# Optimization experiments

Measured on AMD Instinct MI355X. Metric: run time of the kernel, lower is better.

The kernel has to match this reference:

```python
import jax, jax.numpy as jnp
import numpy as np

RNN = 1024     # rnn_size
POSE = 135     # config.pose_size (15 joints x 3x3 rotmat)
SEED = 120     # seed_seq_len
TGT = 24       # target_seq_len
B = 256        # batch size


def setup_inputs() -> dict:
    key = jax.random.key(0)
    k0, k1, k2, k3, k4 = jax.random.split(key, 5)
    s = 1.0 / np.sqrt(RNN)
    poses = jax.random.normal(k0, (B, SEED + TGT, POSE), dtype=jnp.float32)
    # nn.LSTMCell(input_size, rnn_size, bias=False): weights U(-1/sqrt(H), 1/sqrt(H))
    W_ih = jax.random.uniform(k1, (4 * RNN, POSE), minval=-s, maxval=s, dtype=jnp.float32)
    W_hh = jax.random.uniform(k2, (4 * RNN, RNN), minval=-s, maxval=s, dtype=jnp.float32)
    # nn.Linear(rnn_size, pose_size)
    W_fc = jax.random.uniform(k3, (POSE, RNN), minval=-s, maxval=s, dtype=jnp.float32)
    b_fc = jax.random.uniform(k4, (POSE,), minval=-s, maxval=s, dtype=jnp.float32)
    return {"poses": poses, "W_ih": W_ih, "W_hh": W_hh, "W_fc": W_fc, "b_fc": b_fc}


def reference(poses, W_ih, W_hh, W_fc, b_fc):
    def cell(x, h, c):
        # PyTorch LSTMCell gate order: i, f, g, o ; bias=False
        gates = x @ W_ih.T + h @ W_hh.T          # [B, 4*RNN]
        i, f, g, o = jnp.split(gates, 4, axis=-1)
        c_new = jax.nn.sigmoid(f) * c + jax.nn.sigmoid(i) * jnp.tanh(g)
        h_new = jax.nn.sigmoid(o) * jnp.tanh(c_new)
        return h_new, c_new

    # Encoder: steps over poses[:, 0:SEED-1] (dropout p=0 -> identity)
    enc_inputs = jnp.transpose(poses[:, : SEED - 1], (1, 0, 2))  # [SEED-1, B, POSE]
    h0 = jnp.zeros((B, RNN), dtype=poses.dtype)
    c0 = jnp.zeros((B, RNN), dtype=poses.dtype)

    def enc_step(carry, x):
        h, c = carry
        h, c = cell(x, h, c)
        return (h, c), None

    (h, c), _ = jax.lax.scan(enc_step, (h0, c0), enc_inputs)

    # first decoder input (poses[:, SEED-1]) is ground truth. inp is detached.
    inp0 = poses[:, SEED - 1]  # [B, POSE]

    def dec_step(carry, _):
        h, c, inp = carry
        inp = jax.lax.stop_gradient(inp)  # inp.detach() in the original
        h, c = cell(inp, h, c)
        out = inp + h @ W_fc.T + b_fc     # residual + linear decode
        return (h, c, out), out

    _, outs = jax.lax.scan(dec_step, (h, c, inp0), None, length=TGT)  # [TGT, B, POSE]
    return jnp.transpose(outs, (1, 0, 2))  # predictions [B, TGT, POSE]
```

## Files before the change

### kernel.cpp

```cpp
#include <hip/hip_runtime.h>
#include <stdint.h>

#define NB 256
#define NH 1024
#define NPOSE 135
#define NPPAD 160
#define NSTEPS 143
#define NDEC 24
#define KTOT 1184
#define LSTR 168
#define NWG 256

typedef __bf16 bf16;
typedef __attribute__((ext_vector_type(8))) __bf16 bf16x8;
typedef __attribute__((ext_vector_type(4))) float f32x4;
typedef __attribute__((ext_vector_type(4))) uint32_t u32x4;

#define WCAT_OFF 0
#define WCAT_BYTES (4096l * KTOT * 2)
#define WFC_OFF  (WCAT_OFF + WCAT_BYTES)
#define WFC_BYTES (144l * 1024 * 2)
#define X_OFF    (WFC_OFF + WFC_BYTES)
#define X_BYTES  (143l * NB * NPPAD * 2)
#define H_OFF    (X_OFF + X_BYTES)
#define H_BYTES2    (2l * NB * NH * 2)
#define H_BYTES144  (144l * NB * NH * 2)
#define BAR_BYTES 16384

__device__ __forceinline__ u32x4 llc_ld16(const void* p) {
  u32x4 v;
  asm volatile("global_load_dwordx4 %0, %1, off sc0 sc1"
               : "=v"(v) : "v"(p) : "memory");
  return v;
}
__device__ __forceinline__ uint32_t llc_ld4(const void* p) {
  uint32_t v;
  asm volatile("global_load_dword %0, %1, off sc0 sc1"
               : "=v"(v) : "v"(p) : "memory");
  return v;
}
__device__ __forceinline__ u32x4 g_ld16(const void* p) {
  u32x4 v;
  asm volatile("global_load_dwordx4 %0, %1, off"
               : "=v"(v) : "v"(p) : "memory");
  return v;
}
__device__ __forceinline__ u32x4 ld16sel(const void* p, bool cached) {
  return cached ? g_ld16(p) : llc_ld16(p);
}
__device__ __forceinline__ void llc_st2(void* p, uint32_t v) {
  asm volatile("global_store_short %0, %1, off sc0 sc1"
               :: "v"(p), "v"(v) : "memory");
}
#define WAIT_VM(n) do { \
    asm volatile("s_waitcnt vmcnt(" #n ")" ::: "memory"); \
    __builtin_amdgcn_sched_barrier(0); } while (0)

#define POLL(ptr, tgt) do { \
    while (__hip_atomic_load((ptr), __ATOMIC_RELAXED, __HIP_MEMORY_SCOPE_AGENT) < (tgt)) \
      __builtin_amdgcn_s_sleep(1); \
  } while (0)
#define POLL_ALL8(tgt) do { \
    for (;;) { \
      int v_ = __hip_atomic_load(&bar[(bb * 8 + (lane & 7)) * 32], \
                                 __ATOMIC_RELAXED, __HIP_MEMORY_SCOPE_AGENT); \
      if (__all(v_ >= (tgt))) break; \
      __builtin_amdgcn_s_sleep(1); \
    } } while (0)
#define POLL01(tgt) do { \
    for (;;) { \
      int v_ = __hip_atomic_load(&bar[(bb * 8 + (lane & 1)) * 32], \
                                 __ATOMIC_RELAXED, __HIP_MEMORY_SCOPE_AGENT); \
      if (__all(v_ >= (tgt))) break; \
      __builtin_amdgcn_s_sleep(1); \
    } } while (0)
#define CHK(fv, ch, tgt) do { \
    while ((int)(fv) < (tgt)) { \
      __builtin_amdgcn_s_sleep(1); \
      fv = llc_ld4(&bar[(bb * 8 + (ch)) * 32]); \
      WAIT_VM(0); \
    } } while (0)

__global__ void k_zero(uint32_t* p, int n) {
  int i = blockIdx.x * blockDim.x + threadIdx.x;
  int st = gridDim.x * blockDim.x;
  for (; i < n; i += st) p[i] = 0u;
}

__global__ void k_wcat(const float* __restrict__ Whh, const float* __restrict__ Wih,
                       bf16* __restrict__ W) {
  int n = blockIdx.x;
  for (int kk = threadIdx.x; kk < KTOT; kk += blockDim.x) {
    float v = 0.f;
    if (kk < NH) v = Whh[(size_t)n * NH + kk];
    else if (kk - NH < NPOSE) v = Wih[(size_t)n * NPOSE + (kk - NH)];
    W[(size_t)n * KTOT + kk] = (bf16)v;
  }
}

__global__ void k_wfc(const float* __restrict__ Wfc, bf16* __restrict__ W) {
  int p = blockIdx.x;
  for (int kk = threadIdx.x; kk < NH; kk += blockDim.x) {
    float v = (p < NPOSE) ? Wfc[(size_t)p * NH + kk] : 0.f;
    W[(size_t)p * NH + kk] = (bf16)v;
  }
}

__global__ void k_x(const float* __restrict__ poses, bf16* __restrict__ X) {
  int idx = blockIdx.x;
  int t = idx >> 8, b = idx & 255;
  int p = threadIdx.x;
  if (p < NPPAD) {
    float v = (p < NPOSE) ? poses[((size_t)b * 144 + t) * NPOSE + p] : 0.f;
    X[(size_t)idx * NPPAD + p] = (bf16)v;
  }
}

__device__ __forceinline__ float sigm(float x) { return 1.f / (1.f + __expf(-x)); }
__device__ __forceinline__ float tanh_(float x) {
  float e = __expf(2.f * x);
  return 1.f - 2.f / (e + 1.f);
}

template <bool DEEP>
__global__ __launch_bounds__(256, 1) void
k_main(const float* __restrict__ poses, const float* __restrict__ bfc,
       const bf16* __restrict__ Wcat, const bf16* __restrict__ Wfcb,
       bf16* __restrict__ X, bf16* __restrict__ H, int* __restrict__ bar,
       float* __restrict__ out) {
  __shared__ bf16 BldsH[8 * 64 * 128];
  __shared__ bf16 BldsX[64 * LSTR];

  const int tid  = threadIdx.x;
  const int lane = tid & 63;
  const int wv   = tid >> 6;
  const int cl   = lane & 15;
  const int quad = lane >> 4;
  const int L    = blockIdx.x;
  const int jb = (L & 7) * 8 + ((L >> 3) & 7);
  const int bb = L >> 6;
  const int b0 = bb * 64;
  const int j0 = jb * 16;
  const int mych = jb >> 3;
  const bool is_out = ((L & 7) == 7) && (((L >> 3) & 7) < 4);
  const int brow0 = bb * 64 + ((L >> 3) & 7) * 16;

  for (int t = tid; t < 8 * 64 * 16; t += 256) {
    int c = t >> 10, rem = t & 1023, r = rem >> 4, xb = rem & 15;
    u32x4 v = *(const u32x4*)&Wcat[(size_t)((r >> 4) * NH + j0 + (r & 15)) * KTOT
                                   + c * 128 + xb * 8];
    *(u32x4*)&BldsH[(c * 64 + r) * 128 + ((xb ^ (r & 15)) << 3)] = v;
  }
  for (int it = 0; it < 5; ++it) {
    int u = tid + it * 256, r = u / 20, iu = u % 20;
    u32x4 v = *(const u32x4*)&Wcat[(size_t)((r >> 4) * NH + j0 + (r & 15)) * KTOT
                                   + 1024 + iu * 8];
    *(u32x4*)&BldsX[r * LSTR + iu * 8] = v;
  }
  __syncthreads();

  const int arow = b0 + wv * 16 + cl;
  const size_t aBase  = (size_t)arow * NH + quad * 8;
  const size_t axBase = (size_t)arow * NPPAD + quad * 8;

  u32x4 A0[4], A1[4], A2[4], AX[5];
  uint32_t f2 = 0, f3 = 0, f4 = 0, f5 = 0, f6 = 0, f7 = 0;
  f32x4 acc[4];
  float cst[4] = {0.f, 0.f, 0.f, 0.f};

#define FLAGP(ch) (&bar[(bb * 8 + (ch)) * 32])
#define ISSUE_AH(SET, HP, chn) do { \
    const bf16* ga_ = (HP) + aBase + (chn) * 128; \
    SET[0] = ld16sel(ga_, DEEP);      SET[1] = ld16sel(ga_ + 32, DEEP); \
    SET[2] = ld16sel(ga_ + 64, DEEP); SET[3] = ld16sel(ga_ + 96, DEEP); } while (0)
#define ISSUE_AX(sv) do { \
    const bf16* ga_ = X + (size_t)(sv) * NB * NPPAD + axBase; \
    if ((sv) < 120) { \
      AX[0] = g_ld16(ga_);        AX[1] = g_ld16(ga_ + 32); \
      AX[2] = g_ld16(ga_ + 64);   AX[3] = g_ld16(ga_ + 96); \
      AX[4] = g_ld16(ga_ + 128); \
    } else { \
      AX[0] = ld16sel(ga_, DEEP);       AX[1] = ld16sel(ga_ + 32, DEEP); \
      AX[2] = ld16sel(ga_ + 64, DEEP);  AX[3] = ld16sel(ga_ + 96, DEEP); \
      AX[4] = ld16sel(ga_ + 128, DEEP); \
    } } while (0)
#define MFMA_LDS(SET, c) do { \
    _Pragma("unroll") \
    for (int ks = 0; ks < 4; ++ks) { \
      bf16x8 af_ = __builtin_bit_cast(bf16x8, SET[ks]); \
      _Pragma("unroll") \
      for (int gb = 0; gb < 4; ++gb) { \
        bf16x8 bw_ = *(const bf16x8*)&BldsH[((c) * 64 + gb * 16 + cl) * 128 \
                                            + (((ks * 4 + quad) ^ cl) << 3)]; \
        acc[gb] = __builtin_amdgcn_mfma_f32_16x16x32_bf16(af_, bw_, acc[gb], 0, 0, 0); \
      } } } while (0)
#define MFMA_X() do { \
    _Pragma("unroll") \
    for (int ks = 0; ks < 5; ++ks) { \
      bf16x8 af_ = __builtin_bit_cast(bf16x8, AX[ks]); \
      _Pragma("unroll") \
      for (int gb = 0; gb < 4; ++gb) { \
        bf16x8 bw_ = *(const bf16x8*)&BldsX[(gb * 16 + cl) * LSTR + ks * 32 + quad * 8]; \
        acc[gb] = __builtin_amdgcn_mfma_f32_16x16x32_bf16(af_, bw_, acc[gb], 0, 0, 0); \
      } } } while (0)

  ISSUE_AH(A0, H, 0);  f2 = llc_ld4(FLAGP(2));
  ISSUE_AH(A1, H, 1);  f3 = llc_ld4(FLAGP(3));

  for (int s = 0; s < NSTEPS; ++s) {
    const bf16* Hr = H + (size_t)(DEEP ? s : (s & 1)) * (NB * NH);
    bf16* Hw = H + (size_t)(DEEP ? (s + 1) : ((s + 1) & 1)) * (NB * NH);
    #pragma unroll
    for (int gb = 0; gb < 4; ++gb) acc[gb] = f32x4{0, 0, 0, 0};
    const int tgt = 8 * s;

    WAIT_VM(5); CHK(f2, 2, tgt); ISSUE_AH(A2, Hr, 2); f4 = llc_ld4(FLAGP(4)); MFMA_LDS(A0, 0);
    WAIT_VM(5); CHK(f3, 3, tgt); ISSUE_AH(A0, Hr, 3); f5 = llc_ld4(FLAGP(5)); MFMA_LDS(A1, 1);
    WAIT_VM(5); CHK(f4, 4, tgt); ISSUE_AH(A1, Hr, 4); f6 = llc_ld4(FLAGP(6)); MFMA_LDS(A2, 2);
    WAIT_VM(5); CHK(f5, 5, tgt); ISSUE_AH(A2, Hr, 5); f7 = llc_ld4(FLAGP(7)); MFMA_LDS(A0, 3);
    WAIT_VM(5); CHK(f6, 6, tgt); ISSUE_AH(A0, Hr, 6);                         MFMA_LDS(A1, 4);
    WAIT_VM(4); CHK(f7, 7, tgt); ISSUE_AH(A1, Hr, 7);                         MFMA_LDS(A2, 5);
    WAIT_VM(4);
    if (s >= 120) POLL(&bar[(32 + bb) * 32], 4 * (s - 119));
    ISSUE_AX(s);                                               MFMA_LDS(A0, 6);
    WAIT_VM(5);                                                MFMA_LDS(A1, 7);
    WAIT_VM(0);                                                MFMA_X();

    #pragma unroll
    for (int r = 0; r < 4; ++r) {
      float gi = sigm(acc[0][r]);
      float gf = sigm(acc[1][r]);
      float gg = tanh_(acc[2][r]);
      float go = sigm(acc[3][r]);
      float cn = gf * cst[r] + gi * gg;
      cst[r] = cn;
      float h = go * tanh_(cn);
      bf16 hb = (bf16)h;
      llc_st2(&Hw[(size_t)(b0 + wv * 16 + quad * 4 + r) * NH + j0 + cl],
              (uint32_t)__builtin_bit_cast(uint16_t, hb));
    }
    WAIT_VM(0);
    __syncthreads();
    if (tid == 0) atomicAdd(&bar[(bb * 8 + mych) * 32], 1);

    if (s >= 119 && is_out) {
      const int k = s - 119;
      POLL_ALL8(8 * (s + 1));
      f32x4 oa[3] = {{0,0,0,0},{0,0,0,0},{0,0,0,0}};
      const bf16* hrow = Hw + (size_t)(brow0 + cl) * NH;
      for (int kb = 0; kb < 4; ++kb) {
        u32x4 hv[8];
        #pragma unroll
        for (int t = 0; t < 8; ++t)
          hv[t] = ld16sel(&hrow[(kb * 8 + t) * 32 + quad * 8], DEEP);
        WAIT_VM(0);
        #pragma unroll
        for (int t = 0; t < 8; ++t) {
          bf16x8 af = __builtin_bit_cast(bf16x8, hv[t]);
          #pragma unroll
          for (int i = 0; i < 3; ++i) {
            int ct = wv + i * 4;
            if (ct > 8) continue;
            bf16x8 bw = *(const bf16x8*)&Wfcb[(size_t)(ct * 16 + cl) * NH
                                              + (kb * 8 + t) * 32 + quad * 8];
            oa[i] = __builtin_amdgcn_mfma_f32_16x16x32_bf16(af, bw, oa[i], 0, 0, 0);
          }
        }
      }
      #pragma unroll
      for (int i = 0; i < 3; ++i) {
        int ct = wv + i * 4;
        if (ct > 8) continue;
        int p = ct * 16 + cl;
        if (p < NPOSE) {
          #pragma unroll
          for (int r = 0; r < 4; ++r) {
            int b = brow0 + quad * 4 + r;
            float inp = (k == 0) ? poses[((size_t)b * 144 + 119) * NPOSE + p]
                                 : out[((size_t)b * NDEC + (k - 1)) * NPOSE + p];
            float v = oa[i][r] + inp + bfc[p];
            out[((size_t)b * NDEC + k) * NPOSE + p] = v;
            if (s + 1 < NSTEPS) {
              bf16 xb = (bf16)v;
              llc_st2(&X[((size_t)(s + 1) * NB + b) * NPPAD + p],
                      (uint32_t)__builtin_bit_cast(uint16_t, xb));
            }
          }
        }
      }
      if (s + 1 < NSTEPS) {
        WAIT_VM(0);
        __syncthreads();
        if (tid == 0) atomicAdd(&bar[(32 + bb) * 32], 1);
      }
    }

    if (s + 1 < NSTEPS) {
      if constexpr (DEEP) { POLL01(8 * (s + 1)); }
      else                { POLL_ALL8(8 * (s + 1)); }
      ISSUE_AH(A0, Hw, 0);  f2 = llc_ld4(FLAGP(2));
      ISSUE_AH(A1, Hw, 1);  f3 = llc_ld4(FLAGP(3));
    }
  }
}

extern "C" void kernel_launch(void* const* d_in, const int* in_sizes, int n_in,
                              void* d_out, int out_size, void* d_ws, size_t ws_size,
                              hipStream_t stream) {
  const float* poses = (const float*)d_in[0];
  const float* Wih   = (const float*)d_in[1];
  const float* Whh   = (const float*)d_in[2];
  const float* Wfc   = (const float*)d_in[3];
  const float* bfc   = (const float*)d_in[4];

  const size_t need_deep = (size_t)H_OFF + H_BYTES144 + BAR_BYTES;
  const size_t need_min  = (size_t)H_OFF + H_BYTES2 + BAR_BYTES;
  if (ws_size < need_min) return;
  const bool deep = ws_size >= need_deep;
  const size_t hbytes = deep ? (size_t)H_BYTES144 : (size_t)H_BYTES2;

  char* ws = (char*)d_ws;
  bf16* Wcat = (bf16*)(ws + WCAT_OFF);
  bf16* Wfcb = (bf16*)(ws + WFC_OFF);
  bf16* X    = (bf16*)(ws + X_OFF);
  bf16* H    = (bf16*)(ws + H_OFF);
  int*  bar  = (int*)(ws + H_OFF + hbytes);

  if (deep) {
    k_zero<<<256, 256, 0, stream>>>((uint32_t*)(ws + H_OFF), (int)(NB * NH * 2 / 4));
    k_zero<<<32, 256, 0, stream>>>((uint32_t*)bar, BAR_BYTES / 4);
  } else {
    k_zero<<<256, 256, 0, stream>>>((uint32_t*)(ws + H_OFF),
                                    (int)((H_BYTES2 + BAR_BYTES) / 4));
  }
  k_zero<<<256, 256, 0, stream>>>((uint32_t*)(X + (size_t)120 * NB * NPPAD),
                                  (int)(23l * NB * NPPAD * 2 / 4));
  k_wcat<<<4096, 256, 0, stream>>>(Whh, Wih, Wcat);
  k_wfc<<<144, 256, 0, stream>>>(Wfc, Wfcb);
  k_x<<<120 * 256, 256, 0, stream>>>(poses, X);
  if (deep)
    k_main<true><<<NWG, 256, 0, stream>>>(poses, bfc, Wcat, Wfcb, X, H, bar,
                                          (float*)d_out);
  else
    k_main<false><<<NWG, 256, 0, stream>>>(poses, bfc, Wcat, Wfcb, X, H, bar,
                                           (float*)d_out);
}
```

Measured before the change: 1.558 ms.

## Retile per-wave MFMA work to 2x2 blocks with shuffled gate exchange

Each wave now computes a 32-row by 32-column gate tile as a 2x2 grid of 16x16 MFMAs instead of one 16-row strip across all four gates. Each A fragment and each LDS B fragment is reused twice, so LDS reads per MFMA drop. The gate values are then exchanged across lanes with shuffles to form i/f/g/o. It also tracks whether a flag spin already drained the memory counter and skips the partial waits in that case. The cost is double the A-register footprint (loads of H rows per wave) and extra shuffles in the epilogue.

Result: slower. 2.096 ms (+34.5%).

```diff
diff --git a/kernel.cpp b/kernel.cpp
--- a/kernel.cpp
+++ b/kernel.cpp
@@ -55,6 +55,8 @@
 #define WAIT_VM(n) do { \
     asm volatile("s_waitcnt vmcnt(" #n ")" ::: "memory"); \
     __builtin_amdgcn_sched_barrier(0); } while (0)
+#define WAIT_VMC(n) do { \
+    if (__builtin_expect(drained, 0)) { WAIT_VM(0); } else { WAIT_VM(n); } } while (0)
 
 #define POLL(ptr, tgt) do { \
     while (__hip_atomic_load((ptr), __ATOMIC_RELAXED, __HIP_MEMORY_SCOPE_AGENT) < (tgt)) \
@@ -74,8 +76,9 @@
       if (__all(v_ >= (tgt))) break; \
       __builtin_amdgcn_s_sleep(1); \
     } } while (0)
-#define CHK(fv, ch, tgt) do { \
+#define CHKD(fv, ch, tgt) do { \
     while ((int)(fv) < (tgt)) { \
+      drained = true; \
       __builtin_amdgcn_s_sleep(1); \
       fv = llc_ld4(&bar[(bb * 8 + (ch)) * 32]); \
       WAIT_VM(0); \
@@ -136,6 +139,8 @@
   const int wv   = tid >> 6;
   const int cl   = lane & 15;
   const int quad = lane >> 4;
+  const int bh   = wv & 1;
+  const int jh   = wv >> 1;
   const int L    = blockIdx.x;
   const int jb = (L & 7) * 8 + ((L >> 3) & 7);
   const int bb = L >> 6;
@@ -159,50 +164,66 @@
   }
   __syncthreads();
 
-  const int arow = b0 + wv * 16 + cl;
-  const size_t aBase  = (size_t)arow * NH + quad * 8;
-  const size_t axBase = (size_t)arow * NPPAD + quad * 8;
-
-  u32x4 A0[4], A1[4], A2[4], AX[5];
+  const size_t aB0 = (size_t)(b0 + bh * 32 + cl) * NH + quad * 8;
+  const size_t aB1 = aB0 + (size_t)16 * NH;
+  const size_t axB0 = (size_t)(b0 + bh * 32 + cl) * NPPAD + quad * 8;
+  const size_t axB1 = axB0 + (size_t)16 * NPPAD;
+  const int swzk  = jh * 8 + (cl & 7);
+  const int rowB0 = ((cl >> 3) * 16) + swzk;
+  const int rowB1 = rowB0 + 32;
+
+  u32x4 A0[8], A1[8], A2[8], AX[10];
   uint32_t f2 = 0, f3 = 0, f4 = 0, f5 = 0, f6 = 0, f7 = 0;
-  f32x4 acc[4];
-  float cst[4] = {0.f, 0.f, 0.f, 0.f};
+  f32x4 acc[2][2];
+  float cst[4];
+  #pragma unroll
+  for (int r = 0; r < 4; ++r) cst[r] = 0.f;
 
 #define FLAGP(ch) (&bar[(bb * 8 + (ch)) * 32])
 #define ISSUE_AH(SET, HP, chn) do { \
-    const bf16* ga_ = (HP) + aBase + (chn) * 128; \
-    SET[0] = ld16sel(ga_, DEEP);      SET[1] = ld16sel(ga_ + 32, DEEP); \
-    SET[2] = ld16sel(ga_ + 64, DEEP); SET[3] = ld16sel(ga_ + 96, DEEP); } while (0)
+    const bf16* g0_ = (HP) + aB0 + (chn) * 128; \
+    const bf16* g1_ = (HP) + aB1 + (chn) * 128; \
+    SET[0] = ld16sel(g0_, DEEP);      SET[1] = ld16sel(g0_ + 32, DEEP); \
+    SET[2] = ld16sel(g0_ + 64, DEEP); SET[3] = ld16sel(g0_ + 96, DEEP); \
+    SET[4] = ld16sel(g1_, DEEP);      SET[5] = ld16sel(g1_ + 32, DEEP); \
+    SET[6] = ld16sel(g1_ + 64, DEEP); SET[7] = ld16sel(g1_ + 96, DEEP); } while (0)
 #define ISSUE_AX(sv) do { \
-    const bf16* ga_ = X + (size_t)(sv) * NB * NPPAD + axBase; \
+    const bf16* g0_ = X + (size_t)(sv) * NB * NPPAD + axB0; \
+    const bf16* g1_ = X + (size_t)(sv) * NB * NPPAD + axB1; \
     if ((sv) < 120) { \
-      AX[0] = g_ld16(ga_);        AX[1] = g_ld16(ga_ + 32); \
-      AX[2] = g_ld16(ga_ + 64);   AX[3] = g_ld16(ga_ + 96); \
-      AX[4] = g_ld16(ga_ + 128); \
+      _Pragma("unroll") \
+      for (int ks_ = 0; ks_ < 5; ++ks_) { AX[ks_] = g_ld16(g0_ + ks_ * 32); \
+                                          AX[5 + ks_] = g_ld16(g1_ + ks_ * 32); } \
     } else { \
-      AX[0] = ld16sel(ga_, DEEP);       AX[1] = ld16sel(ga_ + 32, DEEP); \
-      AX[2] = ld16sel(ga_ + 64, DEEP);  AX[3] = ld16sel(ga_ + 96, DEEP); \
-      AX[4] = ld16sel(ga_ + 128, DEEP); \
+      _Pragma("unroll") \
+      for (int ks_ = 0; ks_ < 5; ++ks_) { AX[ks_] = ld16sel(g0_ + ks_ * 32, DEEP); \
+                                          AX[5 + ks_] = ld16sel(g1_ + ks_ * 32, DEEP); } \
     } } while (0)
 #define MFMA_LDS(SET, c) do { \
     _Pragma("unroll") \
     for (int ks = 0; ks < 4; ++ks) { \
-      bf16x8 af_ = __builtin_bit_cast(bf16x8, SET[ks]); \
-      _Pragma("unroll") \
-      for (int gb = 0; gb < 4; ++gb) { \
-        bf16x8 bw_ = *(const bf16x8*)&BldsH[((c) * 64 + gb * 16 + cl) * 128 \
-                                            + (((ks * 4 + quad) ^ cl) << 3)]; \
-        acc[gb] = __builtin_amdgcn_mfma_f32_16x16x32_bf16(af_, bw_, acc[gb], 0, 0, 0); \
-      } } } while (0)
+      int slot_ = (((ks * 4 + quad) ^ swzk) << 3); \
+      bf16x8 b0_ = *(const bf16x8*)&BldsH[((c) * 64 + rowB0) * 128 + slot_]; \
+      bf16x8 b1_ = *(const bf16x8*)&BldsH[((c) * 64 + rowB1) * 128 + slot_]; \
+      bf16x8 a0_ = __builtin_bit_cast(bf16x8, SET[ks]); \
+      bf16x8 a1_ = __builtin_bit_cast(bf16x8, SET[4 + ks]); \
+      acc[0][0] = __builtin_amdgcn_mfma_f32_16x16x32_bf16(a0_, b0_, acc[0][0], 0, 0, 0); \
+      acc[0][1] = __builtin_amdgcn_mfma_f32_16x16x32_bf16(a0_, b1_, acc[0][1], 0, 0, 0); \
+      acc[1][0] = __builtin_amdgcn_mfma_f32_16x16x32_bf16(a1_, b0_, acc[1][0], 0, 0, 0); \
+      acc[1][1] = __builtin_amdgcn_mfma_f32_16x16x32_bf16(a1_, b1_, acc[1][1], 0, 0, 0); \
+    } } while (0)
 #define MFMA_X() do { \
     _Pragma("unroll") \
     for (int ks = 0; ks < 5; ++ks) { \
-      bf16x8 af_ = __builtin_bit_cast(bf16x8, AX[ks]); \
-      _Pragma("unroll") \
-      for (int gb = 0; gb < 4; ++gb) { \
-        bf16x8 bw_ = *(const bf16x8*)&BldsX[(gb * 16 + cl) * LSTR + ks * 32 + quad * 8]; \
-        acc[gb] = __builtin_amdgcn_mfma_f32_16x16x32_bf16(af_, bw_, acc[gb], 0, 0, 0); \
-      } } } while (0)
+      bf16x8 b0_ = *(const bf16x8*)&BldsX[rowB0 * LSTR + ks * 32 + quad * 8]; \
+      bf16x8 b1_ = *(const bf16x8*)&BldsX[rowB1 * LSTR + ks * 32 + quad * 8]; \
+      bf16x8 a0_ = __builtin_bit_cast(bf16x8, AX[ks]); \
+      bf16x8 a1_ = __builtin_bit_cast(bf16x8, AX[5 + ks]); \
+      acc[0][0] = __builtin_amdgcn_mfma_f32_16x16x32_bf16(a0_, b0_, acc[0][0], 0, 0, 0); \
+      acc[0][1] = __builtin_amdgcn_mfma_f32_16x16x32_bf16(a0_, b1_, acc[0][1], 0, 0, 0); \
+      acc[1][0] = __builtin_amdgcn_mfma_f32_16x16x32_bf16(a1_, b0_, acc[1][0], 0, 0, 0); \
+      acc[1][1] = __builtin_amdgcn_mfma_f32_16x16x32_bf16(a1_, b1_, acc[1][1], 0, 0, 0); \
+    } } while (0)
 
   ISSUE_AH(A0, H, 0);  f2 = llc_ld4(FLAGP(2));
   ISSUE_AH(A1, H, 1);  f3 = llc_ld4(FLAGP(3));
@@ -211,33 +232,50 @@
     const bf16* Hr = H + (size_t)(DEEP ? s : (s & 1)) * (NB * NH);
     bf16* Hw = H + (size_t)(DEEP ? (s + 1) : ((s + 1) & 1)) * (NB * NH);
     #pragma unroll
-    for (int gb = 0; gb < 4; ++gb) acc[gb] = f32x4{0, 0, 0, 0};
+    for (int a = 0; a < 2; ++a)
+      #pragma unroll
+      for (int bt = 0; bt < 2; ++bt) acc[a][bt] = f32x4{0, 0, 0, 0};
     const int tgt = 8 * s;
-
-    WAIT_VM(5); CHK(f2, 2, tgt); ISSUE_AH(A2, Hr, 2); f4 = llc_ld4(FLAGP(4)); MFMA_LDS(A0, 0);
-    WAIT_VM(5); CHK(f3, 3, tgt); ISSUE_AH(A0, Hr, 3); f5 = llc_ld4(FLAGP(5)); MFMA_LDS(A1, 1);
-    WAIT_VM(5); CHK(f4, 4, tgt); ISSUE_AH(A1, Hr, 4); f6 = llc_ld4(FLAGP(6)); MFMA_LDS(A2, 2);
-    WAIT_VM(5); CHK(f5, 5, tgt); ISSUE_AH(A2, Hr, 5); f7 = llc_ld4(FLAGP(7)); MFMA_LDS(A0, 3);
-    WAIT_VM(5); CHK(f6, 6, tgt); ISSUE_AH(A0, Hr, 6);                         MFMA_LDS(A1, 4);
-    WAIT_VM(4); CHK(f7, 7, tgt); ISSUE_AH(A1, Hr, 7);                         MFMA_LDS(A2, 5);
-    WAIT_VM(4);
+    bool drained = false;
+
+    WAIT_VM(9);  CHKD(f2, 2, tgt); ISSUE_AH(A2, Hr, 2); f4 = llc_ld4(FLAGP(4)); MFMA_LDS(A0, 0);
+    WAIT_VMC(9); CHKD(f3, 3, tgt); ISSUE_AH(A0, Hr, 3); f5 = llc_ld4(FLAGP(5)); MFMA_LDS(A1, 1);
+    WAIT_VMC(9); CHKD(f4, 4, tgt); ISSUE_AH(A1, Hr, 4); f6 = llc_ld4(FLAGP(6)); MFMA_LDS(A2, 2);
+    WAIT_VMC(9); CHKD(f5, 5, tgt); ISSUE_AH(A2, Hr, 5); f7 = llc_ld4(FLAGP(7)); MFMA_LDS(A0, 3);
+    WAIT_VMC(9); CHKD(f6, 6, tgt); ISSUE_AH(A0, Hr, 6);                         MFMA_LDS(A1, 4);
+    WAIT_VMC(8); CHKD(f7, 7, tgt); ISSUE_AH(A1, Hr, 7);                         MFMA_LDS(A2, 5);
+    WAIT_VMC(8);
     if (s >= 120) POLL(&bar[(32 + bb) * 32], 4 * (s - 119));
     ISSUE_AX(s);                                               MFMA_LDS(A0, 6);
-    WAIT_VM(5);                                                MFMA_LDS(A1, 7);
-    WAIT_VM(0);                                                MFMA_X();
-
-    #pragma unroll
-    for (int r = 0; r < 4; ++r) {
-      float gi = sigm(acc[0][r]);
-      float gf = sigm(acc[1][r]);
-      float gg = tanh_(acc[2][r]);
-      float go = sigm(acc[3][r]);
-      float cn = gf * cst[r] + gi * gg;
-      cst[r] = cn;
-      float h = go * tanh_(cn);
-      bf16 hb = (bf16)h;
-      llc_st2(&Hw[(size_t)(b0 + wv * 16 + quad * 4 + r) * NH + j0 + cl],
-              (uint32_t)__builtin_bit_cast(uint16_t, hb));
+    WAIT_VMC(10);                                              MFMA_LDS(A1, 7);
+    WAIT_VMC(0);                                               MFMA_X();
+
+    {
+      const bool hi = (cl & 8) != 0;
+      #pragma unroll
+      for (int a = 0; a < 2; ++a) {
+        float s0[4], s1[4];
+        #pragma unroll
+        for (int e = 0; e < 4; ++e) {
+          s0[e] = __shfl_xor(acc[a][0][e], 8);
+          s1[e] = __shfl_xor(acc[a][1][e], 8);
+        }
+        #pragma unroll
+        for (int rr = 0; rr < 2; ++rr) {
+          int r = hi ? (2 + rr) : rr;
+          float iv = hi ? s0[r] : acc[a][0][r];
+          float fv = hi ? acc[a][0][r] : s0[r];
+          float gv = hi ? s1[r] : acc[a][1][r];
+          float ov = hi ? acc[a][1][r] : s1[r];
+          float cn = sigm(fv) * cst[a * 2 + rr] + sigm(iv) * tanh_(gv);
+          cst[a * 2 + rr] = cn;
+          float h = sigm(ov) * tanh_(cn);
+          bf16 hb = (bf16)h;
+          llc_st2(&Hw[(size_t)(b0 + bh * 32 + a * 16 + quad * 4 + r) * NH
+                      + j0 + jh * 8 + (cl & 7)],
+                  (uint32_t)__builtin_bit_cast(uint16_t, hb));
+        }
+      }
     }
     WAIT_VM(0);
     __syncthreads();
```
